# Optimization experiments

Measured on AMD Instinct MI355X. Metric: run time of the kernel, lower is better.

Reference implementation:

```python
import jax, jax.numpy as jnp
import numpy as np

N_NODES = 100000
N_EDGES = 1600000
IN_CH, HID_CH, OUT_CH = 64, 128, 128


def setup_inputs() -> dict:
    key = jax.random.key(0)
    ks = jax.random.split(key, 10)
    x = jax.random.normal(ks[0], (N_NODES, IN_CH), dtype=jnp.float32)
    edge_index = jax.random.randint(ks[1], (2, N_EDGES), 0, N_NODES, dtype=jnp.int64 if jax.config.jax_enable_x64 else jnp.int32)
    edge_weight = jax.random.uniform(ks[2], (N_EDGES,), dtype=jnp.float32)
    def glorot(k, fan_in, fan_out):
        lim = np.sqrt(6.0 / (fan_in + fan_out)).astype(np.float32)
        return jax.random.uniform(k, (fan_in, fan_out), minval=-lim, maxval=lim, dtype=jnp.float32)
    W1 = glorot(ks[3], IN_CH, HID_CH)
    b1 = jnp.zeros((HID_CH,), jnp.float32)
    W2 = glorot(ks[4], HID_CH, HID_CH)
    b2 = jnp.zeros((HID_CH,), jnp.float32)
    W3 = glorot(ks[5], HID_CH, OUT_CH)
    b3 = jnp.zeros((OUT_CH,), jnp.float32)
    return {"x": x, "edge_index": edge_index, "edge_weight": edge_weight,
            "W1": W1, "b1": b1, "W2": W2, "b2": b2, "W3": W3, "b3": b3}


def _gcn_norm(edge_index, edge_weight, num_nodes):
    # add self-loops with weight 1 (PyG GCNConv default)
    loop = jnp.arange(num_nodes, dtype=edge_index.dtype)
    src = jnp.concatenate([edge_index[0], loop])
    dst = jnp.concatenate([edge_index[1], loop])
    w = jnp.concatenate([edge_weight, jnp.ones((num_nodes,), edge_weight.dtype)])
    deg = jax.ops.segment_sum(w, dst, num_segments=num_nodes)
    dinv = jnp.where(deg > 0, jax.lax.rsqrt(deg), 0.0)
    norm = dinv[src] * w * dinv[dst]
    return src, dst, norm


def _gcn_layer(x, W, b, src, dst, norm, num_nodes):
    h = x @ W                                  # [N, C_out]
    msg = h[src] * norm[:, None]               # gather + scale, [E+N, C_out]
    agg = jax.ops.segment_sum(msg, dst, num_segments=num_nodes)
    return agg + b


def reference(x, edge_index, edge_weight, W1, b1, W2, b2, W3, b3):
    n = x.shape[0]
    src, dst, norm = _gcn_norm(edge_index, edge_weight, n)
    h = jax.nn.silu(_gcn_layer(x, W1, b1, src, dst, norm, n))
    h = jax.nn.silu(_gcn_layer(h, W2, b2, src, dst, norm, n))
    h = jax.nn.silu(_gcn_layer(h, W3, b3, src, dst, norm, n))
    # single-graph global mean pool (batch == zeros)
    return jnp.mean(h, axis=0, keepdims=True)  # [1, out_channels]
```

## Files before the change

### kernel.cpp

```cpp
#include <hip/hip_runtime.h>

#define C 128
#define INCH 64
#define FIXP 33554432.0f

typedef unsigned short bf16_t;
typedef unsigned char fp8_t;
typedef float f32x4 __attribute__((ext_vector_type(4)));
typedef float f32x2 __attribute__((ext_vector_type(2)));
typedef unsigned int u32x4 __attribute__((ext_vector_type(4)));

__device__ __forceinline__ float silu_f(float v) {
    return v / (1.0f + __expf(-v));
}

__device__ __forceinline__ bf16_t f2bf(float f) {
    unsigned b = __float_as_uint(f);
    return (bf16_t)((b + 0x7FFFu + ((b >> 16) & 1u)) >> 16);
}
__device__ __forceinline__ float bf2f(unsigned u) {
    return __uint_as_float(u << 16);
}

__device__ __forceinline__ fp8_t f2fp8(float f) {
    unsigned b = __float_as_uint(f);
    unsigned s = (b >> 24) & 0x80u;
    unsigned a = b & 0x7FFFFFFFu;
    if (a >= 0x43E00000u) return (fp8_t)(s | 0x7E);
    int e = (int)(a >> 23);
    int e8 = e - 120;
    if (e8 <= 0) {
        float av = __uint_as_float(a);
        int q = (int)(av * 512.0f + 0.5f);
        if (q > 8) q = 8;
        return (fp8_t)(s | (unsigned)q);
    }
    unsigned m = a & 0x7FFFFFu;
    unsigned m3 = m >> 20;
    unsigned rest = m & 0xFFFFFu;
    if (rest > 0x80000u || (rest == 0x80000u && (m3 & 1u))) m3++;
    unsigned enc = ((unsigned)e8 << 3) + m3;
    if (enc >= 0x7Fu) enc = 0x7Eu;
    return (fp8_t)(s | enc);
}
__device__ __forceinline__ float fp82f(unsigned v) {
    unsigned s = (v & 0x80u) << 24;
    unsigned e = (v >> 3) & 0xFu;
    unsigned m = v & 7u;
    if (e) return __uint_as_float(s | ((e + 120u) << 23) | (m << 20));
    float f = (float)m * 0.001953125f;
    return __uint_as_float(s | __float_as_uint(f));
}
__device__ __forceinline__ float4 dec4(unsigned v) {
#if __has_builtin(__builtin_amdgcn_cvt_pk_f32_fp8)
    f32x2 lo = __builtin_amdgcn_cvt_pk_f32_fp8((int)v, false);
    f32x2 hi = __builtin_amdgcn_cvt_pk_f32_fp8((int)v, true);
    return make_float4(lo[0], lo[1], hi[0], hi[1]);
#else
    return make_float4(fp82f(v & 0xFFu), fp82f((v >> 8) & 0xFFu),
                       fp82f((v >> 16) & 0xFFu), fp82f(v >> 24));
#endif
}
__device__ __forceinline__ float2 dec2(unsigned v) {
#if __has_builtin(__builtin_amdgcn_cvt_pk_f32_fp8)
    f32x2 lo = __builtin_amdgcn_cvt_pk_f32_fp8((int)v, false);
    return make_float2(lo[0], lo[1]);
#else
    return make_float2(fp82f(v & 0xFFu), fp82f((v >> 8) & 0xFFu));
#endif
}

__device__ __forceinline__ void mfma16x16x32(f32x4& d, u32x4 a, u32x4 b) {
    asm("v_mfma_f32_16x16x32_bf16 %0, %1, %2, %0" : "+v"(d) : "v"(a), "v"(b));
}


template<int NCH> struct VecN;
template<> struct VecN<4> { using T = float4; };
template<> struct VecN<2> { using T = float2; };

template<int NCH> struct Ld8;
template<> struct Ld8<4> {
    static __device__ __forceinline__ float4 ld(const fp8_t* p) {
        return dec4(*(const unsigned*)p);
    }
};
template<> struct Ld8<2> {
    static __device__ __forceinline__ float2 ld(const fp8_t* p) {
        return dec2((unsigned)*(const unsigned short*)p);
    }
};

template<int NCH> struct StB;
template<> struct StB<4> {
    static __device__ __forceinline__ void st(bf16_t* p, float4 v) {
        *(ushort4*)p = make_ushort4(f2bf(v.x), f2bf(v.y), f2bf(v.z), f2bf(v.w));
    }
};
template<> struct StB<2> {
    static __device__ __forceinline__ void st(bf16_t* p, float2 v) {
        *(ushort2*)p = make_ushort2(f2bf(v.x), f2bf(v.y));
    }
};

__device__ __forceinline__ float4 vfma(const float4 v, float n, float4 a) {
    a.x = fmaf(v.x, n, a.x); a.y = fmaf(v.y, n, a.y);
    a.z = fmaf(v.z, n, a.z); a.w = fmaf(v.w, n, a.w); return a;
}
__device__ __forceinline__ float2 vfma(const float2 v, float n, float2 a) {
    a.x = fmaf(v.x, n, a.x); a.y = fmaf(v.y, n, a.y); return a;
}
__device__ __forceinline__ float4 vmul(const float4 v, float s) {
    return make_float4(v.x * s, v.y * s, v.z * s, v.w * s);
}
__device__ __forceinline__ float2 vmul(const float2 v, float s) {
    return make_float2(v.x * s, v.y * s);
}
__device__ __forceinline__ float4 vadd(const float4 a, const float4 b) {
    return make_float4(a.x + b.x, a.y + b.y, a.z + b.z, a.w + b.w);
}
__device__ __forceinline__ float2 vadd(const float2 a, const float2 b) {
    return make_float2(a.x + b.x, a.y + b.y);
}


__global__ void hist_k(const int* __restrict__ dst, const float* __restrict__ w,
                       unsigned long long* packed, int* __restrict__ rank, int E) {
    int e = blockIdx.x * blockDim.x + threadIdx.x;
    if (e < E) {
        unsigned fx = (unsigned)(w[e] * FIXP + 0.5f);
        unsigned long long old =
            atomicAdd(&packed[dst[e]], (1ull << 32) | (unsigned long long)fx);
        rank[e] = (int)(old >> 32);
    }
}


__global__ void cvt_fp8_k(const float* __restrict__ in, const float* __restrict__ dinv,
                          fp8_t* __restrict__ out, int n4) {
    int i = blockIdx.x * blockDim.x + threadIdx.x;
    if (i < n4) {
        float dv = dinv[i >> 4];
        float4 v = *(const float4*)&in[(size_t)i * 4];
        uchar4 u = make_uchar4(f2fp8(v.x * dv), f2fp8(v.y * dv),
                               f2fp8(v.z * dv), f2fp8(v.w * dv));
        *(uchar4*)&out[(size_t)i * 4] = u;
    }
}


__global__ void wfrag_k(const float* __restrict__ W, bf16_t* __restrict__ Wf, int K) {
    int idx = blockIdx.x * blockDim.x + threadIdx.x;
    if (idx >= K * 128) return;
    int KS = K / 32;
    int j = idx & 7;
    int lane = (idx >> 3) & 63;
    int rest = idx >> 9;
    int ks = rest % KS;
    int nt = rest / KS;
    int col = nt * 16 + (lane & 15);
    int k = ks * 32 + (lane >> 4) * 8 + j;
    Wf[idx] = f2bf(W[k * 128 + col]);
}


#define SCAN_T 256
#define SCAN_E 1024

__global__ void scan1_k(const unsigned long long* __restrict__ packed,
                        int* rowptr, int* bsums, float* __restrict__ dinv, int N) {
    __shared__ int s[SCAN_T];
    int t = threadIdx.x;
    int base = blockIdx.x * SCAN_E + t * 4;
    int v[4];
    #pragma unroll
    for (int j = 0; j < 4; ++j) {
        int i = base + j;
        if (i < N) {
            unsigned long long p = packed[i];
            v[j] = (int)(p >> 32);
            float deg = 1.0f + (float)(unsigned)(p & 0xffffffffull) * (1.0f / FIXP);
            dinv[i] = rsqrtf(deg);
        } else v[j] = 0;
    }
    int sum = v[0] + v[1] + v[2] + v[3];
    s[t] = sum; __syncthreads();
    for (int off = 1; off < SCAN_T; off <<= 1) {
        int y = (t >= off) ? s[t - off] : 0;
        __syncthreads();
        s[t] += y;
        __syncthreads();
    }
    int incl = s[t];
    int excl = incl - sum;
    if (t == SCAN_T - 1) bsums[blockIdx.x] = incl;
    int run = excl;
    #pragma unroll
    for (int j = 0; j < 4; ++j) { int i = base + j; if (i < N) rowptr[i] = run; run += v[j]; }
}

__global__ void scan2_k(int* bsums, int nb) {
    __shared__ int s[128];
    int t = threadIdx.x;
    int v = (t < nb) ? bsums[t] : 0;
    s[t] = v; __syncthreads();
    for (int off = 1; off < 128; off <<= 1) {
        int y = (t >= off) ? s[t - off] : 0;
        __syncthreads();
        s[t] += y;
        __syncthreads();
    }
    if (t < nb) bsums[t] = s[t] - v;
}

__global__ void scan3_k(int* rowptr, const int* __restrict__ bsums, int N, int E) {
    int i = blockIdx.x * blockDim.x + threadIdx.x;
    if (i < N) rowptr[i] += bsums[i >> 10];
    if (i == 0) rowptr[N] = E;
}


__global__ void fill_csr_k(const int* __restrict__ src, const int* __restrict__ dst,
                           const float* __restrict__ w,
                           const int* __restrict__ rowptr, const int* __restrict__ rank,
                           unsigned* edata, int E) {
    int e = blockIdx.x * blockDim.x + threadIdx.x;
    if (e >= E) return;
    int pos = rowptr[dst[e]] + rank[e];
    edata[pos] = ((unsigned)src[e] << 15) | (unsigned)f2bf(w[e]);
}


template<int CH>
__launch_bounds__(256)
__global__ void agg_gather_k(const fp8_t* __restrict__ Xin, const unsigned* __restrict__ edata,
                             const int* __restrict__ rowptr, const float* __restrict__ dinv,
                             bf16_t* __restrict__ outbuf, int N) {
    constexpr int NCH = CH / 32;
    using VecT = typename VecN<NCH>::T;
    const int g = threadIdx.x >> 5;
    const int l = threadIdx.x & 31;
    const int d = blockIdx.x * 8 + g;
    if (d >= N) return;
    const int c = l * NCH;

    float di = dinv[d];
    VecT a0 = Ld8<NCH>::ld(&Xin[(size_t)d * CH + c]);
    VecT a1 = {}, a2 = {}, a3 = {};
    const int beg = rowptr[d], end = rowptr[d + 1];
    for (int j = beg; j < end; j += 4) {
        int j1 = j + 1, j2 = j + 2, j3 = j + 3;
        unsigned m0 = edata[j];
        unsigned m1 = edata[j1 < end ? j1 : j];
        unsigned m2 = edata[j2 < end ? j2 : j];
        unsigned m3 = edata[j3 < end ? j3 : j];
        float n0 = bf2f(m0 & 0x7FFFu);
        float n1 = j1 < end ? bf2f(m1 & 0x7FFFu) : 0.f;
        float n2 = j2 < end ? bf2f(m2 & 0x7FFFu) : 0.f;
        float n3 = j3 < end ? bf2f(m3 & 0x7FFFu) : 0.f;
        VecT v0 = Ld8<NCH>::ld(&Xin[(size_t)(m0 >> 15) * CH + c]);
        VecT v1 = Ld8<NCH>::ld(&Xin[(size_t)(m1 >> 15) * CH + c]);
        VecT v2 = Ld8<NCH>::ld(&Xin[(size_t)(m2 >> 15) * CH + c]);
        VecT v3 = Ld8<NCH>::ld(&Xin[(size_t)(m3 >> 15) * CH + c]);
        a0 = vfma(v0, n0, a0);
        a1 = vfma(v1, n1, a1);
        a2 = vfma(v2, n2, a2);
        a3 = vfma(v3, n3, a3);
    }
    VecT acc = vmul(vadd(vadd(a0, a1), vadd(a2, a3)), di);
    StB<NCH>::st(&outbuf[(size_t)d * CH + c], acc);
}


template<int K, bool POOL>
__launch_bounds__(256)
__global__ void gemm_mfma_k(const bf16_t* __restrict__ A, const bf16_t* __restrict__ Wf,
                            const float* __restrict__ bias, const float* __restrict__ dinv,
                            void* __restrict__ outp, int N) {
    constexpr int KS = K / 32;
    const int tid = threadIdx.x;
    const int wid = tid >> 6;
    const int lane = tid & 63;
    const int r0 = blockIdx.x * 64 + wid * 16;
    const int col = lane & 15;
    const int kgrp = lane >> 4;

    int arow = r0 + col;
    if (arow > N - 1) arow = N - 1;

    f32x4 acc[8] = {};
    #pragma unroll
    for (int ks = 0; ks < KS; ++ks) {
        u32x4 a = *(const u32x4*)(A + (size_t)arow * K + ks * 32 + kgrp * 8);
        #pragma unroll
        for (int n = 0; n < 8; ++n) {
            u32x4 b = *(const u32x4*)(Wf + ((size_t)(n * KS + ks) * 64 + lane) * 8);
            mfma16x16x32(acc[n], a, b);
        }
    }

    const int rbase = r0 + kgrp * 4;
    if (!POOL) {
        fp8_t* out = (fp8_t*)outp;
        float dv[4];
        #pragma unroll
        for (int j = 0; j < 4; ++j) {
            int r = rbase + j;
            dv[j] = (r < N) ? dinv[r] : 0.f;
        }
        #pragma unroll
        for (int n = 0; n < 8; ++n) {
            float bc = bias[n * 16 + col];
            #pragma unroll
            for (int j = 0; j < 4; ++j) {
                int r = rbase + j;
                if (r < N)
                    out[(size_t)r * C + n * 16 + col] = f2fp8(silu_f(acc[n][j] + bc) * dv[j]);
            }
        }
    } else {
        float s[8];
        #pragma unroll
        for (int n = 0; n < 8; ++n) {
            float bc = bias[n * 16 + col];
            float t = 0.f;
            #pragma unroll
            for (int j = 0; j < 4; ++j) {
                int r = rbase + j;
                float v = silu_f(acc[n][j] + bc);
                t += (r < N) ? v : 0.f;
            }
            s[n] = t;
        }
        #pragma unroll
        for (int n = 0; n < 8; ++n) {
            s[n] += __shfl_xor(s[n], 16);
            s[n] += __shfl_xor(s[n], 32);
        }
        __shared__ float part[4][C];
        if (lane < 16) {
            #pragma unroll
            for (int n = 0; n < 8; ++n) part[wid][n * 16 + lane] = s[n];
        }
        __syncthreads();
        if (tid < C) {
            float t = part[0][tid] + part[1][tid] + part[2][tid] + part[3][tid];
            ((float*)outp)[(size_t)blockIdx.x * C + tid] = t;
        }
    }
}


__global__ void reduce1_k(const float* __restrict__ partial, float* __restrict__ p2,
                          int NB, int chunk) {
    int t = threadIdx.x;
    int r0 = blockIdx.x * chunk;
    int r1 = r0 + chunk; if (r1 > NB) r1 = NB;
    float s = 0.f;
    for (int r = r0; r < r1; ++r) s += partial[(size_t)r * C + t];
    p2[(size_t)blockIdx.x * C + t] = s;
}

__global__ void reduce2_k(const float* __restrict__ p2, float* __restrict__ out,
                          int R1, float inv_n) {
    int t = threadIdx.x;
    float s = 0.f;
    for (int r = 0; r < R1; ++r) s += p2[(size_t)r * C + t];
    out[t] = s * inv_n;
}


extern "C" void kernel_launch(void* const* d_in, const int* in_sizes, int n_in,
                              void* d_out, int out_size, void* d_ws, size_t ws_size,
                              hipStream_t stream) {
    const float* x  = (const float*)d_in[0];
    const int*   ei = (const int*)d_in[1];
    const float* ew = (const float*)d_in[2];
    const float* W1 = (const float*)d_in[3];
    const float* b1 = (const float*)d_in[4];
    const float* W2 = (const float*)d_in[5];
    const float* b2 = (const float*)d_in[6];
    const float* W3 = (const float*)d_in[7];
    const float* b3 = (const float*)d_in[8];
    float* out = (float*)d_out;

    const int N = in_sizes[0] / INCH;
    const int E = in_sizes[1] / 2;
    const int* src = ei;
    const int* dst = ei + E;

    char* ws = (char*)d_ws;
    size_t off = 0;
    auto alloc = [&](size_t bytes) -> void* {
        void* p = ws + off;
        off += (bytes + 255) & ~(size_t)255;
        return p;
    };
    bf16_t*   A      = (bf16_t*)  alloc((size_t)N * C * sizeof(bf16_t));
    fp8_t*    Xh8    = (fp8_t*)   alloc((size_t)N * C);
    fp8_t*    x8     = (fp8_t*)   alloc((size_t)N * INCH);
    unsigned* edata  = (unsigned*)alloc((size_t)E * sizeof(unsigned));
    int*      rank   = (int*)     alloc((size_t)E * sizeof(int));
    int*      rowptr = (int*)     alloc((size_t)(N + 1) * sizeof(int));
    unsigned long long* packed = (unsigned long long*)alloc((size_t)N * 8);
    float*    dinv   = (float*)   alloc((size_t)N * sizeof(float));
    int*      bsums  = (int*)     alloc(256 * sizeof(int));
    float*    p2     = (float*)   alloc(64 * C * sizeof(float));
    bf16_t*   Wf1    = (bf16_t*)  alloc((size_t)INCH * C * sizeof(bf16_t));
    bf16_t*   Wf2    = (bf16_t*)  alloc((size_t)C * C * sizeof(bf16_t));
    bf16_t*   Wf3    = (bf16_t*)  alloc((size_t)C * C * sizeof(bf16_t));
    (void)ws_size;

    const int nb = (N + 255) / 256;
    const int eb = (E + 255) / 256;
    const int sbk = (N + SCAN_E - 1) / SCAN_E;

    hipMemsetAsync(packed, 0, (size_t)N * 8, stream);
    hist_k<<<eb, 256, 0, stream>>>(dst, ew, packed, rank, E);
    scan1_k<<<sbk, SCAN_T, 0, stream>>>(packed, rowptr, bsums, dinv, N);
    scan2_k<<<1, 128, 0, stream>>>(bsums, sbk);
    scan3_k<<<nb, 256, 0, stream>>>(rowptr, bsums, N, E);
    fill_csr_k<<<eb, 256, 0, stream>>>(src, dst, ew, rowptr, rank, edata, E);
    const int cv4 = (N * INCH) / 4;
    cvt_fp8_k<<<(cv4 + 255) / 256, 256, 0, stream>>>(x, dinv, x8, cv4);
    wfrag_k<<<(INCH * C + 255) / 256, 256, 0, stream>>>(W1, Wf1, INCH);
    wfrag_k<<<(C * C + 255) / 256, 256, 0, stream>>>(W2, Wf2, C);
    wfrag_k<<<(C * C + 255) / 256, 256, 0, stream>>>(W3, Wf3, C);

    const int ab  = (N + 7) / 8;
    const int gb2 = (N + 63) / 64;

    agg_gather_k<INCH><<<ab, 256, 0, stream>>>(x8, edata, rowptr, dinv, A, N);
    gemm_mfma_k<INCH, false><<<gb2, 256, 0, stream>>>(A, Wf1, b1, dinv, Xh8, N);
    agg_gather_k<C><<<ab, 256, 0, stream>>>(Xh8, edata, rowptr, dinv, A, N);
    gemm_mfma_k<C, false><<<gb2, 256, 0, stream>>>(A, Wf2, b2, dinv, Xh8, N);
    agg_gather_k<C><<<ab, 256, 0, stream>>>(Xh8, edata, rowptr, dinv, A, N);
    float* partial = (float*)x8;
    gemm_mfma_k<C, true><<<gb2, 256, 0, stream>>>(A, Wf3, b3, dinv, partial, N);

    const int R1 = 64;
    const int chunk = (gb2 + R1 - 1) / R1;
    reduce1_k<<<R1, 128, 0, stream>>>(partial, p2, gb2, chunk);
    reduce2_k<<<1, 128, 0, stream>>>(p2, out, R1, 1.0f / (float)N);
}
```

Measured before the change: 334.1 us.

## Merge weight-prep and scan kernels, pack dst with rank, widen per-thread gather

```diff
diff --git a/kernel.cpp b/kernel.cpp
--- a/kernel.cpp
+++ b/kernel.cpp
@@ -61,77 +61,44 @@
                        fp82f((v >> 16) & 0xFFu), fp82f(v >> 24));
 #endif
 }
-__device__ __forceinline__ float2 dec2(unsigned v) {
-#if __has_builtin(__builtin_amdgcn_cvt_pk_f32_fp8)
-    f32x2 lo = __builtin_amdgcn_cvt_pk_f32_fp8((int)v, false);
-    return make_float2(lo[0], lo[1]);
-#else
-    return make_float2(fp82f(v & 0xFFu), fp82f((v >> 8) & 0xFFu));
-#endif
-}
 
 __device__ __forceinline__ void mfma16x16x32(f32x4& d, u32x4 a, u32x4 b) {
     asm("v_mfma_f32_16x16x32_bf16 %0, %1, %2, %0" : "+v"(d) : "v"(a), "v"(b));
 }
 
 
-template<int NCH> struct VecN;
-template<> struct VecN<4> { using T = float4; };
-template<> struct VecN<2> { using T = float2; };
-
-template<int NCH> struct Ld8;
-template<> struct Ld8<4> {
-    static __device__ __forceinline__ float4 ld(const fp8_t* p) {
-        return dec4(*(const unsigned*)p);
-    }
-};
-template<> struct Ld8<2> {
-    static __device__ __forceinline__ float2 ld(const fp8_t* p) {
-        return dec2((unsigned)*(const unsigned short*)p);
-    }
-};
-
-template<int NCH> struct StB;
-template<> struct StB<4> {
-    static __device__ __forceinline__ void st(bf16_t* p, float4 v) {
-        *(ushort4*)p = make_ushort4(f2bf(v.x), f2bf(v.y), f2bf(v.z), f2bf(v.w));
-    }
-};
-template<> struct StB<2> {
-    static __device__ __forceinline__ void st(bf16_t* p, float2 v) {
-        *(ushort2*)p = make_ushort2(f2bf(v.x), f2bf(v.y));
-    }
-};
+template<int NV>
+__device__ __forceinline__ void ld_dec(const fp8_t* p, float4* o) {
+    if constexpr (NV == 1) {
+        o[0] = dec4(*(const unsigned*)p);
+    } else {
+        uint2 u = *(const uint2*)p;
+        o[0] = dec4(u.x);
+        o[1] = dec4(u.y);
+    }
+}
 
 __device__ __forceinline__ float4 vfma(const float4 v, float n, float4 a) {
     a.x = fmaf(v.x, n, a.x); a.y = fmaf(v.y, n, a.y);
     a.z = fmaf(v.z, n, a.z); a.w = fmaf(v.w, n, a.w); return a;
 }
-__device__ __forceinline__ float2 vfma(const float2 v, float n, float2 a) {
-    a.x = fmaf(v.x, n, a.x); a.y = fmaf(v.y, n, a.y); return a;
-}
 __device__ __forceinline__ float4 vmul(const float4 v, float s) {
     return make_float4(v.x * s, v.y * s, v.z * s, v.w * s);
 }
-__device__ __forceinline__ float2 vmul(const float2 v, float s) {
-    return make_float2(v.x * s, v.y * s);
-}
 __device__ __forceinline__ float4 vadd(const float4 a, const float4 b) {
     return make_float4(a.x + b.x, a.y + b.y, a.z + b.z, a.w + b.w);
 }
-__device__ __forceinline__ float2 vadd(const float2 a, const float2 b) {
-    return make_float2(a.x + b.x, a.y + b.y);
-}
 
 
 __global__ void hist_k(const int* __restrict__ dst, const float* __restrict__ w,
-                       unsigned long long* packed, int* __restrict__ rank, int E) {
+                       unsigned long long* packed, unsigned* __restrict__ dstrank, int E) {
     int e = blockIdx.x * blockDim.x + threadIdx.x;
     if (e < E) {
+        int d = dst[e];
         unsigned fx = (unsigned)(w[e] * FIXP + 0.5f);
         unsigned long long old =
-            atomicAdd(&packed[dst[e]], (1ull << 32) | (unsigned long long)fx);
-        rank[e] = (int)(old >> 32);
+            atomicAdd(&packed[d], (1ull << 32) | (unsigned long long)fx);
+        dstrank[e] = ((unsigned)d << 15) | (unsigned)(old >> 32);
     }
 }
 
@@ -149,18 +116,25 @@
 }
 
 
-__global__ void wfrag_k(const float* __restrict__ W, bf16_t* __restrict__ Wf, int K) {
-    int idx = blockIdx.x * blockDim.x + threadIdx.x;
-    if (idx >= K * 128) return;
+__device__ __forceinline__ void wfrag_one(const float* W, bf16_t* Wf, int id, int K) {
     int KS = K / 32;
-    int j = idx & 7;
-    int lane = (idx >> 3) & 63;
-    int rest = idx >> 9;
+    int j = id & 7;
+    int lane = (id >> 3) & 63;
+    int rest = id >> 9;
     int ks = rest % KS;
     int nt = rest / KS;
     int col = nt * 16 + (lane & 15);
     int k = ks * 32 + (lane >> 4) * 8 + j;
-    Wf[idx] = f2bf(W[k * 128 + col]);
+    Wf[id] = f2bf(W[k * 128 + col]);
+}
+
+__global__ void wfrag3_k(const float* __restrict__ W1, const float* __restrict__ W2,
+                         const float* __restrict__ W3, bf16_t* Wf1, bf16_t* Wf2, bf16_t* Wf3) {
+    int idx = blockIdx.x * blockDim.x + threadIdx.x;
+    const int n1 = INCH * C, n2 = C * C;
+    if (idx < n1)                wfrag_one(W1, Wf1, idx, INCH);
+    else if (idx < n1 + n2)      wfrag_one(W2, Wf2, idx - n1, C);
+    else if (idx < n1 + 2 * n2)  wfrag_one(W3, Wf3, idx - n1 - n2, C);
 }
 
 
@@ -199,34 +173,26 @@
     for (int j = 0; j < 4; ++j) { int i = base + j; if (i < N) rowptr[i] = run; run += v[j]; }
 }
 
-__global__ void scan2_k(int* bsums, int nb) {
-    __shared__ int s[128];
-    int t = threadIdx.x;
-    int v = (t < nb) ? bsums[t] : 0;
-    s[t] = v; __syncthreads();
-    for (int off = 1; off < 128; off <<= 1) {
-        int y = (t >= off) ? s[t - off] : 0;
-        __syncthreads();
-        s[t] += y;
-        __syncthreads();
-    }
-    if (t < nb) bsums[t] = s[t] - v;
-}
 
 __global__ void scan3_k(int* rowptr, const int* __restrict__ bsums, int N, int E) {
     int i = blockIdx.x * blockDim.x + threadIdx.x;
-    if (i < N) rowptr[i] += bsums[i >> 10];
+    if (i < N) {
+        int bucket = i >> 10;
+        int off = 0;
+        for (int b = 0; b < bucket; ++b) off += bsums[b];
+        rowptr[i] += off;
+    }
     if (i == 0) rowptr[N] = E;
 }
 
 
-__global__ void fill_csr_k(const int* __restrict__ src, const int* __restrict__ dst,
-                           const float* __restrict__ w,
-                           const int* __restrict__ rowptr, const int* __restrict__ rank,
+__global__ void fill_csr_k(const int* __restrict__ src, const float* __restrict__ w,
+                           const int* __restrict__ rowptr, const unsigned* __restrict__ dstrank,
                            unsigned* edata, int E) {
     int e = blockIdx.x * blockDim.x + threadIdx.x;
     if (e >= E) return;
-    int pos = rowptr[dst[e]] + rank[e];
+    unsigned dr = dstrank[e];
+    int pos = rowptr[dr >> 15] + (int)(dr & 0x7FFFu);
     edata[pos] = ((unsigned)src[e] << 15) | (unsigned)f2bf(w[e]);
 }
 
@@ -236,17 +202,22 @@
 __global__ void agg_gather_k(const fp8_t* __restrict__ Xin, const unsigned* __restrict__ edata,
                              const int* __restrict__ rowptr, const float* __restrict__ dinv,
                              bf16_t* __restrict__ outbuf, int N) {
-    constexpr int NCH = CH / 32;
-    using VecT = typename VecN<NCH>::T;
-    const int g = threadIdx.x >> 5;
-    const int l = threadIdx.x & 31;
-    const int d = blockIdx.x * 8 + g;
+    constexpr int NCH = CH / 16;
+    constexpr int NV  = NCH / 4;
+    const int g = threadIdx.x >> 4;
+    const int l = threadIdx.x & 15;
+    const int d = blockIdx.x * 16 + g;
     if (d >= N) return;
     const int c = l * NCH;
 
     float di = dinv[d];
-    VecT a0 = Ld8<NCH>::ld(&Xin[(size_t)d * CH + c]);
-    VecT a1 = {}, a2 = {}, a3 = {};
+    float4 a0[NV], a1[NV], a2[NV], a3[NV];
+    ld_dec<NV>(&Xin[(size_t)d * CH + c], a0);
+    #pragma unroll
+    for (int q = 0; q < NV; ++q) {
+        a1[q] = make_float4(0.f, 0.f, 0.f, 0.f);
+        a2[q] = a1[q]; a3[q] = a1[q];
+    }
     const int beg = rowptr[d], end = rowptr[d + 1];
     for (int j = beg; j < end; j += 4) {
         int j1 = j + 1, j2 = j + 2, j3 = j + 3;
@@ -258,17 +229,25 @@
         float n1 = j1 < end ? bf2f(m1 & 0x7FFFu) : 0.f;
         float n2 = j2 < end ? bf2f(m2 & 0x7FFFu) : 0.f;
         float n3 = j3 < end ? bf2f(m3 & 0x7FFFu) : 0.f;
-        VecT v0 = Ld8<NCH>::ld(&Xin[(size_t)(m0 >> 15) * CH + c]);
-        VecT v1 = Ld8<NCH>::ld(&Xin[(size_t)(m1 >> 15) * CH + c]);
-        VecT v2 = Ld8<NCH>::ld(&Xin[(size_t)(m2 >> 15) * CH + c]);
-        VecT v3 = Ld8<NCH>::ld(&Xin[(size_t)(m3 >> 15) * CH + c]);
-        a0 = vfma(v0, n0, a0);
-        a1 = vfma(v1, n1, a1);
-        a2 = vfma(v2, n2, a2);
-        a3 = vfma(v3, n3, a3);
-    }
-    VecT acc = vmul(vadd(vadd(a0, a1), vadd(a2, a3)), di);
-    StB<NCH>::st(&outbuf[(size_t)d * CH + c], acc);
+        float4 v0[NV], v1[NV], v2[NV], v3[NV];
+        ld_dec<NV>(&Xin[(size_t)(m0 >> 15) * CH + c], v0);
+        ld_dec<NV>(&Xin[(size_t)(m1 >> 15) * CH + c], v1);
+        ld_dec<NV>(&Xin[(size_t)(m2 >> 15) * CH + c], v2);
+        ld_dec<NV>(&Xin[(size_t)(m3 >> 15) * CH + c], v3);
+        #pragma unroll
+        for (int q = 0; q < NV; ++q) {
+            a0[q] = vfma(v0[q], n0, a0[q]);
+            a1[q] = vfma(v1[q], n1, a1[q]);
+            a2[q] = vfma(v2[q], n2, a2[q]);
+            a3[q] = vfma(v3[q], n3, a3[q]);
+        }
+    }
+    #pragma unroll
+    for (int q = 0; q < NV; ++q) {
+        float4 acc = vmul(vadd(vadd(a0[q], a1[q]), vadd(a2[q], a3[q])), di);
+        *(ushort4*)&outbuf[(size_t)d * CH + c + q * 4] =
+            make_ushort4(f2bf(acc.x), f2bf(acc.y), f2bf(acc.z), f2bf(acc.w));
+    }
 }
 
 
@@ -396,19 +375,19 @@
         off += (bytes + 255) & ~(size_t)255;
         return p;
     };
-    bf16_t*   A      = (bf16_t*)  alloc((size_t)N * C * sizeof(bf16_t));
-    fp8_t*    Xh8    = (fp8_t*)   alloc((size_t)N * C);
-    fp8_t*    x8     = (fp8_t*)   alloc((size_t)N * INCH);
-    unsigned* edata  = (unsigned*)alloc((size_t)E * sizeof(unsigned));
-    int*      rank   = (int*)     alloc((size_t)E * sizeof(int));
-    int*      rowptr = (int*)     alloc((size_t)(N + 1) * sizeof(int));
+    bf16_t*   A       = (bf16_t*)  alloc((size_t)N * C * sizeof(bf16_t));
+    fp8_t*    Xh8     = (fp8_t*)   alloc((size_t)N * C);
+    fp8_t*    x8      = (fp8_t*)   alloc((size_t)N * INCH);
+    unsigned* edata   = (unsigned*)alloc((size_t)E * sizeof(unsigned));
+    unsigned* dstrank = (unsigned*)alloc((size_t)E * sizeof(unsigned));
+    int*      rowptr  = (int*)     alloc((size_t)(N + 1) * sizeof(int));
     unsigned long long* packed = (unsigned long long*)alloc((size_t)N * 8);
-    float*    dinv   = (float*)   alloc((size_t)N * sizeof(float));
-    int*      bsums  = (int*)     alloc(256 * sizeof(int));
-    float*    p2     = (float*)   alloc(64 * C * sizeof(float));
-    bf16_t*   Wf1    = (bf16_t*)  alloc((size_t)INCH * C * sizeof(bf16_t));
-    bf16_t*   Wf2    = (bf16_t*)  alloc((size_t)C * C * sizeof(bf16_t));
-    bf16_t*   Wf3    = (bf16_t*)  alloc((size_t)C * C * sizeof(bf16_t));
+    float*    dinv    = (float*)   alloc((size_t)N * sizeof(float));
+    int*      bsums   = (int*)     alloc(256 * sizeof(int));
+    float*    p2      = (float*)   alloc(64 * C * sizeof(float));
+    bf16_t*   Wf1     = (bf16_t*)  alloc((size_t)INCH * C * sizeof(bf16_t));
+    bf16_t*   Wf2     = (bf16_t*)  alloc((size_t)C * C * sizeof(bf16_t));
+    bf16_t*   Wf3    = (bf16_t*)   alloc((size_t)C * C * sizeof(bf16_t));
     (void)ws_size;
 
     const int nb = (N + 255) / 256;
@@ -416,18 +395,16 @@
     const int sbk = (N + SCAN_E - 1) / SCAN_E;
 
     hipMemsetAsync(packed, 0, (size_t)N * 8, stream);
-    hist_k<<<eb, 256, 0, stream>>>(dst, ew, packed, rank, E);
+    hist_k<<<eb, 256, 0, stream>>>(dst, ew, packed, dstrank, E);
     scan1_k<<<sbk, SCAN_T, 0, stream>>>(packed, rowptr, bsums, dinv, N);
-    scan2_k<<<1, 128, 0, stream>>>(bsums, sbk);
     scan3_k<<<nb, 256, 0, stream>>>(rowptr, bsums, N, E);
-    fill_csr_k<<<eb, 256, 0, stream>>>(src, dst, ew, rowptr, rank, edata, E);
+    fill_csr_k<<<eb, 256, 0, stream>>>(src, ew, rowptr, dstrank, edata, E);
     const int cv4 = (N * INCH) / 4;
     cvt_fp8_k<<<(cv4 + 255) / 256, 256, 0, stream>>>(x, dinv, x8, cv4);
-    wfrag_k<<<(INCH * C + 255) / 256, 256, 0, stream>>>(W1, Wf1, INCH);
-    wfrag_k<<<(C * C + 255) / 256, 256, 0, stream>>>(W2, Wf2, C);
-    wfrag_k<<<(C * C + 255) / 256, 256, 0, stream>>>(W3, Wf3, C);
-
-    const int ab  = (N + 7) / 8;
+    const int wtot = INCH * C + 2 * C * C;
+    wfrag3_k<<<(wtot + 255) / 256, 256, 0, stream>>>(W1, W2, W3, Wf1, Wf2, Wf3);
+
+    const int ab  = (N + 15) / 16;
     const int gb2 = (N + 63) / 64;
 
     agg_gather_k<INCH><<<ab, 256, 0, stream>>>(x8, edata, rowptr, dinv, A, N);
```

Measured after the change: 312.2 us. 6.5% less time.
